# Optimization experiments

Hardware: AMD Instinct MI355X
Metric: run time of the kernel (lower is better)

## Reference

```python
import jax, jax.numpy as jnp
import numpy as np

N_NODES = 100000
N_EDGES = 4000000
CHANNELS = 64


def setup_inputs() -> dict:
    key = jax.random.key(0)
    k1, k2, k3, k4, k5 = jax.random.split(key, 5)
    x = jax.random.normal(k1, (N_NODES, CHANNELS), dtype=jnp.float32)
    sources = jax.random.randint(k2, (N_EDGES,), 0, N_NODES, dtype=jnp.int64)
    targets = jax.random.randint(k3, (N_EDGES,), 0, N_NODES, dtype=jnp.int64)
    norm = jax.random.uniform(k4, (N_NODES, 1), dtype=jnp.float32)
    # xavier_normal_ for a (64, 64) weight: std = sqrt(2 / (fan_in + fan_out))
    std = float(np.sqrt(2.0 / (CHANNELS + CHANNELS)))
    weight = jax.random.normal(k5, (CHANNELS, CHANNELS), dtype=jnp.float32) * std
    return {"x": x, "sources": sources, "targets": targets, "norm": norm, "weight": weight}


def reference(x, sources, targets, norm, weight):
    # x.index_add(0, targets, x[sources]) == x + segment_sum(x[sources], targets)
    messages = x[sources]  # [E, C] gather
    agg = x + jax.ops.segment_sum(messages, targets, num_segments=x.shape[0])  # [N, C]
    h = norm * agg  # per-node scale, norm broadcasts [N,1] over [N,C]
    return h @ weight  # [N, C]
```

## Files before the change

kernel.cpp:

```cpp
#include <hip/hip_runtime.h>


constexpr int C = 64;
constexpr int BN = 128;
constexpr int CHUNK2 = 8192;
constexpr int MAXB = 1024;
constexpr int NPASS = 7;
constexpr int BINS = BN * 8;
constexpr int ASTRIDE = 65;
constexpr int UNI = BN * ASTRIDE;
constexpr int TAILCAP = 65536;
constexpr int CSTR = 32;

__global__ __launch_bounds__(256) void init_kernel(
    int* __restrict__ cursor, int* __restrict__ tailcnt, int NB, int slot) {
  int i = blockIdx.x * 256 + threadIdx.x;
  if (i < NB) cursor[i * CSTR] = i * slot;
  if (i == NB) *tailcnt = 0;
}

__global__ __launch_bounds__(512) void binfused_kernel(
    const int* __restrict__ src, const int* __restrict__ tgt,
    int* __restrict__ gcursor, int* __restrict__ tailcnt,
    unsigned* __restrict__ tailrec, unsigned* __restrict__ recs,
    const float* __restrict__ x, unsigned* __restrict__ xb,
    int E, int NB, int slot, int binBlocks, int total8) {
  if ((int)blockIdx.x >= binBlocks) {
    int i = (blockIdx.x - binBlocks) * 512 + threadIdx.x;
    if (i < total8) {
      const float4* x4 = (const float4*)x;
      float4 a = x4[i * 2], bq = x4[i * 2 + 1];
      float f[8] = {a.x, a.y, a.z, a.w, bq.x, bq.y, bq.z, bq.w};
      unsigned w[4];
#pragma unroll
      for (int k = 0; k < 4; k++) {
        unsigned u0 = __float_as_uint(f[2 * k]);
        unsigned u1 = __float_as_uint(f[2 * k + 1]);
        u0 = (u0 + 0x7FFFu + ((u0 >> 16) & 1u)) >> 16;
        u1 = (u1 + 0x7FFFu + ((u1 >> 16) & 1u)) >> 16;
        w[k] = u0 | (u1 << 16);
      }
      ((uint4*)xb)[i] = make_uint4(w[0], w[1], w[2], w[3]);
    }
    return;
  }
  __shared__ unsigned rs[CHUNK2];
  __shared__ unsigned short sb[CHUNK2];
  __shared__ int hist[MAXB];
  __shared__ int gb[MAXB];
  __shared__ int cbase[MAXB];
  __shared__ int pre[512];
  int tid = threadIdx.x;
  int base = blockIdx.x * CHUNK2;
  int count = E - base; if (count > CHUNK2) count = CHUNK2;

  for (int i = tid; i < MAXB; i += 512) hist[i] = 0;
  __syncthreads();

  unsigned mrec[16];
  unsigned mbix[16];
  int nv = count >> 2;
  int rem = count & 3;
  const int4* s4 = (const int4*)(src + base);
  const int4* t4 = (const int4*)(tgt + base);
#pragma unroll
  for (int j = 0; j < 4; j++) {
    int i = tid + j * 512;
    if (i < nv) {
      int4 s = s4[i], t = t4[i];
      int b0 = t.x >> 7, b1 = t.y >> 7, b2 = t.z >> 7, b3 = t.w >> 7;
      mrec[4 * j + 0] = ((unsigned)s.x << 7) | (unsigned)(t.x & 127);
      mrec[4 * j + 1] = ((unsigned)s.y << 7) | (unsigned)(t.y & 127);
      mrec[4 * j + 2] = ((unsigned)s.z << 7) | (unsigned)(t.z & 127);
      mrec[4 * j + 3] = ((unsigned)s.w << 7) | (unsigned)(t.w & 127);
      mbix[4 * j + 0] = ((unsigned)b0 << 13) | (unsigned)atomicAdd(&hist[b0], 1);
      mbix[4 * j + 1] = ((unsigned)b1 << 13) | (unsigned)atomicAdd(&hist[b1], 1);
      mbix[4 * j + 2] = ((unsigned)b2 << 13) | (unsigned)atomicAdd(&hist[b2], 1);
      mbix[4 * j + 3] = ((unsigned)b3 << 13) | (unsigned)atomicAdd(&hist[b3], 1);
    } else {
#pragma unroll
      for (int k = 0; k < 4; k++) mbix[4 * j + k] = 0xFFFFFFFFu;
    }
  }
  unsigned trec = 0, tbix = 0xFFFFFFFFu;
  if (tid < rem) {
    int i = (nv << 2) + tid;
    int s = src[base + i], t = tgt[base + i];
    int b = t >> 7;
    trec = ((unsigned)s << 7) | (unsigned)(t & 127);
    tbix = ((unsigned)b << 13) | (unsigned)atomicAdd(&hist[b], 1);
  }
  __syncthreads();

  int c0 = hist[2 * tid], c1 = hist[2 * tid + 1];
  pre[tid] = c0 + c1;
  __syncthreads();
  for (int off = 1; off < 512; off <<= 1) {
    int v = pre[tid];
    int a = (tid >= off) ? pre[tid - off] : 0;
    __syncthreads();
    pre[tid] = v + a;
    __syncthreads();
  }
  {
    int run = pre[tid] - (c0 + c1);
    cbase[2 * tid] = run;
    cbase[2 * tid + 1] = run + c0;
  }
  if (2 * tid < NB && c0) gb[2 * tid] = atomicAdd(&gcursor[2 * tid * CSTR], c0);
  if (2 * tid + 1 < NB && c1)
    gb[2 * tid + 1] = atomicAdd(&gcursor[(2 * tid + 1) * CSTR], c1);
  __syncthreads();

#pragma unroll
  for (int j = 0; j < 16; j++) {
    unsigned v = mbix[j];
    if (v != 0xFFFFFFFFu) {
      int b = (int)(v >> 13);
      int pos = cbase[b] + (int)(v & 8191u);
      rs[pos] = mrec[j];
      sb[pos] = (unsigned short)b;
    }
  }
  if (tbix != 0xFFFFFFFFu) {
    int b = (int)(tbix >> 13);
    int pos = cbase[b] + (int)(tbix & 8191u);
    rs[pos] = trec;
    sb[pos] = (unsigned short)b;
  }
  __syncthreads();

  for (int i = tid; i < count; i += 512) {
    int b = (int)sb[i];
    int dest = gb[b] + (i - cbase[b]);
    if (dest < (b + 1) * slot) {
      recs[dest] = rs[i];
    } else {
      int tp = atomicAdd(tailcnt, 1);
      if (tp < TAILCAP) {
        tailrec[2 * tp] = rs[i];
        tailrec[2 * tp + 1] = (unsigned)b;
      }
    }
  }
}

__device__ __forceinline__ void acc8_bf16(float (&a)[8], uint4 v) {
  a[0] += __uint_as_float(v.x << 16);
  a[1] += __uint_as_float(v.x & 0xFFFF0000u);
  a[2] += __uint_as_float(v.y << 16);
  a[3] += __uint_as_float(v.y & 0xFFFF0000u);
  a[4] += __uint_as_float(v.z << 16);
  a[5] += __uint_as_float(v.z & 0xFFFF0000u);
  a[6] += __uint_as_float(v.w << 16);
  a[7] += __uint_as_float(v.w & 0xFFFF0000u);
}

__device__ __forceinline__ void acc8_f32(float (&a)[8], float4 u, float4 v) {
  a[0] += u.x; a[1] += u.y; a[2] += u.z; a[3] += u.w;
  a[4] += v.x; a[5] += v.y; a[6] += v.z; a[7] += v.w;
}

template <bool USE_BF16>
__global__ __launch_bounds__(512) void sortgather_kernel(
    const float* __restrict__ x, const unsigned* __restrict__ xb,
    const unsigned* __restrict__ recs, const int* __restrict__ cursor,
    const int* __restrict__ tailcnt, const unsigned* __restrict__ tailrec,
    const float* __restrict__ norm, const float* __restrict__ W,
    float* __restrict__ out, int N, int slot) {
  __shared__ int cnt[BINS];
  __shared__ int pre[512];
  __shared__ int nst[BINS + 1];
  __shared__ float uni[UNI];
  unsigned* sorted = (unsigned*)uni;
  float* accum = uni;
  int tid = threadIdx.x;
  int lane = tid & 63;
  int wave = tid >> 6;
  int b = blockIdx.x;
  int n0 = b * BN;
  int nn = N - n0; if (nn > BN) nn = BN;
  int beg = b * slot;
  int m = cursor[b * CSTR] - beg; if (m > slot) m = slot;
  int end = beg + m;

  unsigned myrec[16];
#pragma unroll
  for (int j = 0; j < 16; j++) {
    int r = beg + tid + j * 512;
    myrec[j] = (r < end) ? recs[r] : 0xFFFFFFFFu;
  }
  cnt[tid] = 0; cnt[tid + 512] = 0;
  __syncthreads();
#pragma unroll
  for (int j = 0; j < 16; j++) {
    unsigned rc = myrec[j];
    if (rc != 0xFFFFFFFFu) {
      int q = (int)(rc >> 21); if (q > 6) q = 6;
      atomicAdd(&cnt[((int)(rc & 127u) << 3) | q], 1);
    }
  }
  __syncthreads();
  int c0 = cnt[2 * tid], c1 = cnt[2 * tid + 1];
  pre[tid] = c0 + c1;
  __syncthreads();
  for (int off = 1; off < 512; off <<= 1) {
    int v = pre[tid];
    int a = (tid >= off) ? pre[tid - off] : 0;
    __syncthreads();
    pre[tid] = v + a;
    __syncthreads();
  }
  {
    int run = pre[tid] - (c0 + c1);
    nst[2 * tid] = run;
    nst[2 * tid + 1] = run + c0;
    cnt[2 * tid] = run;
    cnt[2 * tid + 1] = run + c0;
  }
  if (tid == 0) nst[BINS] = m;
  __syncthreads();
#pragma unroll
  for (int j = 0; j < 16; j++) {
    unsigned rc = myrec[j];
    if (rc != 0xFFFFFFFFu) {
      int q = (int)(rc >> 21); if (q > 6) q = 6;
      int p = atomicAdd(&cnt[((int)(rc & 127u) << 3) | q], 1);
      sorted[p] = rc >> 7;
    }
  }
  __syncthreads();

  int l7 = tid & 7;
  int g  = tid >> 3;
  int k0 = g, k1 = g + 64;
  bool has0 = k0 < nn, has1 = k1 < nn;
  const float4* x4 = (const float4*)x;
  const uint4* xb4 = (const uint4*)xb;

  float a0[8], a1[8];
  if (has0) {
    float4 u = x4[(n0 + k0) * 16 + l7 * 2], v = x4[(n0 + k0) * 16 + l7 * 2 + 1];
    a0[0] = u.x; a0[1] = u.y; a0[2] = u.z; a0[3] = u.w;
    a0[4] = v.x; a0[5] = v.y; a0[6] = v.z; a0[7] = v.w;
  } else {
#pragma unroll
    for (int j = 0; j < 8; j++) a0[j] = 0.0f;
  }
  if (has1) {
    float4 u = x4[(n0 + k1) * 16 + l7 * 2], v = x4[(n0 + k1) * 16 + l7 * 2 + 1];
    a1[0] = u.x; a1[1] = u.y; a1[2] = u.z; a1[3] = u.w;
    a1[4] = v.x; a1[5] = v.y; a1[6] = v.z; a1[7] = v.w;
  } else {
#pragma unroll
    for (int j = 0; j < 8; j++) a1[j] = 0.0f;
  }

  for (int p = 0; p < NPASS; p++) {
    if (has0) {
      int e = nst[k0 * 8 + p], ge = nst[k0 * 8 + p + 1];
      for (; e + 1 < ge; e += 2) {
        int s0 = (int)sorted[e], s1 = (int)sorted[e + 1];
        if (USE_BF16) {
          uint4 v0 = xb4[s0 * 8 + l7];
          uint4 v1 = xb4[s1 * 8 + l7];
          acc8_bf16(a0, v0); acc8_bf16(a0, v1);
        } else {
          float4 u0 = x4[s0 * 16 + l7 * 2], w0 = x4[s0 * 16 + l7 * 2 + 1];
          float4 u1 = x4[s1 * 16 + l7 * 2], w1 = x4[s1 * 16 + l7 * 2 + 1];
          acc8_f32(a0, u0, w0); acc8_f32(a0, u1, w1);
        }
      }
      if (e < ge) {
        int s = (int)sorted[e];
        if (USE_BF16) { uint4 v = xb4[s * 8 + l7]; acc8_bf16(a0, v); }
        else { acc8_f32(a0, x4[s * 16 + l7 * 2], x4[s * 16 + l7 * 2 + 1]); }
      }
    }
    if (has1) {
      int e = nst[k1 * 8 + p], ge = nst[k1 * 8 + p + 1];
      for (; e + 1 < ge; e += 2) {
        int s0 = (int)sorted[e], s1 = (int)sorted[e + 1];
        if (USE_BF16) {
          uint4 v0 = xb4[s0 * 8 + l7];
          uint4 v1 = xb4[s1 * 8 + l7];
          acc8_bf16(a1, v0); acc8_bf16(a1, v1);
        } else {
          float4 u0 = x4[s0 * 16 + l7 * 2], w0 = x4[s0 * 16 + l7 * 2 + 1];
          float4 u1 = x4[s1 * 16 + l7 * 2], w1 = x4[s1 * 16 + l7 * 2 + 1];
          acc8_f32(a1, u0, w0); acc8_f32(a1, u1, w1);
        }
      }
      if (e < ge) {
        int s = (int)sorted[e];
        if (USE_BF16) { uint4 v = xb4[s * 8 + l7]; acc8_bf16(a1, v); }
        else { acc8_f32(a1, x4[s * 16 + l7 * 2], x4[s * 16 + l7 * 2 + 1]); }
      }
    }
  }

  {
    int tc = *tailcnt; if (tc > TAILCAP) tc = TAILCAP;
    for (int r = 0; r < tc; r++) {
      if ((int)tailrec[2 * r + 1] != b) continue;
      unsigned rc = tailrec[2 * r];
      int tl = (int)(rc & 127u);
      if (tl == k0 || tl == k1) {
        int s = (int)(rc >> 7);
        if (USE_BF16) {
          uint4 v = xb4[s * 8 + l7];
          if (tl == k0) acc8_bf16(a0, v); else acc8_bf16(a1, v);
        } else {
          float4 u = x4[s * 16 + l7 * 2], w = x4[s * 16 + l7 * 2 + 1];
          if (tl == k0) acc8_f32(a0, u, w); else acc8_f32(a1, u, w);
        }
      }
    }
  }
  __syncthreads();

  if (has0) {
#pragma unroll
    for (int j = 0; j < 8; j++) accum[k0 * ASTRIDE + 8 * l7 + j] = a0[j];
  }
  if (has1) {
#pragma unroll
    for (int j = 0; j < 8; j++) accum[k1 * ASTRIDE + 8 * l7 + j] = a1[j];
  }
  __syncthreads();

  float wreg[C];
#pragma unroll
  for (int k = 0; k < C; k++) wreg[k] = W[k * C + lane];

  for (int i = wave; i < nn; i += 8) {
    int n = n0 + i;
    float a = accum[i * ASTRIDE + lane];
    float o = 0.0f;
#pragma unroll
    for (int c = 0; c < C; c++)
      o = fmaf(__shfl(a, c, 64), wreg[c], o);
    out[n * C + lane] = o * norm[n];
  }
}

extern "C" void kernel_launch(void* const* d_in, const int* in_sizes, int n_in,
                              void* d_out, int out_size, void* d_ws, size_t ws_size,
                              hipStream_t stream) {
  const float* x       = (const float*)d_in[0];
  const int*   sources = (const int*)d_in[1];
  const int*   targets = (const int*)d_in[2];
  const float* norm    = (const float*)d_in[3];
  const float* weight  = (const float*)d_in[4];
  float* out = (float*)d_out;

  int N = in_sizes[0] / C;
  int E = in_sizes[1];
  int NB = (N + BN - 1) / BN;

  size_t availw = ws_size / 4;
  size_t xw = (size_t)N * C / 2;
  size_t fixedw = (size_t)NB * CSTR + 1 + 2 * (size_t)TAILCAP;
  bool use_bf16; int slot;
  if (availw >= xw + fixedw + (size_t)NB * 8192) { use_bf16 = true; slot = 8192; }
  else if (availw >= xw + fixedw + (size_t)NB * 6144) { use_bf16 = true; slot = 6144; }
  else {
    use_bf16 = false;
    size_t s = (availw > fixedw) ? (availw - fixedw) / (size_t)NB : 0;
    slot = s > 8192 ? 8192 : (int)s;
  }

  unsigned* xb; int* cursor;
  if (use_bf16) {
    xb = (unsigned*)d_ws;
    cursor = (int*)d_ws + xw;
  } else {
    xb = nullptr;
    cursor = (int*)d_ws;
  }
  int* tailcnt = cursor + (size_t)NB * CSTR;
  unsigned* tailrec = (unsigned*)(tailcnt + 1);
  unsigned* recs = tailrec + 2 * (size_t)TAILCAP;

  int hb = (E + CHUNK2 - 1) / CHUNK2;
  int total8 = N * C / 8;
  int cvtBlocks = use_bf16 ? (total8 + 511) / 512 : 0;

  init_kernel<<<(NB + 256) / 256, 256, 0, stream>>>(cursor, tailcnt, NB, slot);
  binfused_kernel<<<hb + cvtBlocks, 512, 0, stream>>>(
      sources, targets, cursor, tailcnt, tailrec, recs, x, xb,
      E, NB, slot, hb, total8);
  if (use_bf16) {
    sortgather_kernel<true><<<NB, 512, 0, stream>>>(
        x, xb, recs, cursor, tailcnt, tailrec, norm, weight, out, N, slot);
  } else {
    sortgather_kernel<false><<<NB, 512, 0, stream>>>(
        x, xb, recs, cursor, tailcnt, tailrec, norm, weight, out, N, slot);
  }
}
```

Measured before the change: 284.0 us.

## Split bf16 convert kernel, scatter bins directly, make sortgather persistent

The bf16 conversion moves out of the fused binning kernel into its own grid-stride kernel. The binning kernel drops its shared-memory local sort and prefix scan and writes each record straight to its global slot, which cuts shared memory and barriers but makes the global writes less coalesced. The sortgather kernel becomes persistent, with 512 blocks looping over the 782 node tiles, which avoids one launch wave of blocks but gives an uneven two-pass tail. It also reloads the weight registers on every iteration.

```diff
diff --git a/kernel.cpp b/kernel.cpp
--- a/kernel.cpp
+++ b/kernel.cpp
@@ -11,6 +11,7 @@
 constexpr int UNI = BN * ASTRIDE;
 constexpr int TAILCAP = 65536;
 constexpr int CSTR = 32;
+constexpr int SGBLK = 512;
 
 __global__ __launch_bounds__(256) void init_kernel(
     int* __restrict__ cursor, int* __restrict__ tailcnt, int NB, int slot) {
@@ -19,37 +20,33 @@
   if (i == NB) *tailcnt = 0;
 }
 
-__global__ __launch_bounds__(512) void binfused_kernel(
+__global__ __launch_bounds__(256) void cvt_kernel(
+    const float* __restrict__ x, unsigned* __restrict__ xb, int total8) {
+  int stride = gridDim.x * 256;
+  for (int i = blockIdx.x * 256 + threadIdx.x; i < total8; i += stride) {
+    const float4* x4 = (const float4*)x;
+    float4 a = x4[i * 2], bq = x4[i * 2 + 1];
+    float f[8] = {a.x, a.y, a.z, a.w, bq.x, bq.y, bq.z, bq.w};
+    unsigned w[4];
+#pragma unroll
+    for (int k = 0; k < 4; k++) {
+      unsigned u0 = __float_as_uint(f[2 * k]);
+      unsigned u1 = __float_as_uint(f[2 * k + 1]);
+      u0 = (u0 + 0x7FFFu + ((u0 >> 16) & 1u)) >> 16;
+      u1 = (u1 + 0x7FFFu + ((u1 >> 16) & 1u)) >> 16;
+      w[k] = u0 | (u1 << 16);
+    }
+    ((uint4*)xb)[i] = make_uint4(w[0], w[1], w[2], w[3]);
+  }
+}
+
+__global__ __launch_bounds__(512) void bin_kernel(
     const int* __restrict__ src, const int* __restrict__ tgt,
     int* __restrict__ gcursor, int* __restrict__ tailcnt,
     unsigned* __restrict__ tailrec, unsigned* __restrict__ recs,
-    const float* __restrict__ x, unsigned* __restrict__ xb,
-    int E, int NB, int slot, int binBlocks, int total8) {
-  if ((int)blockIdx.x >= binBlocks) {
-    int i = (blockIdx.x - binBlocks) * 512 + threadIdx.x;
-    if (i < total8) {
-      const float4* x4 = (const float4*)x;
-      float4 a = x4[i * 2], bq = x4[i * 2 + 1];
-      float f[8] = {a.x, a.y, a.z, a.w, bq.x, bq.y, bq.z, bq.w};
-      unsigned w[4];
-#pragma unroll
-      for (int k = 0; k < 4; k++) {
-        unsigned u0 = __float_as_uint(f[2 * k]);
-        unsigned u1 = __float_as_uint(f[2 * k + 1]);
-        u0 = (u0 + 0x7FFFu + ((u0 >> 16) & 1u)) >> 16;
-        u1 = (u1 + 0x7FFFu + ((u1 >> 16) & 1u)) >> 16;
-        w[k] = u0 | (u1 << 16);
-      }
-      ((uint4*)xb)[i] = make_uint4(w[0], w[1], w[2], w[3]);
-    }
-    return;
-  }
-  __shared__ unsigned rs[CHUNK2];
-  __shared__ unsigned short sb[CHUNK2];
+    int E, int NB, int slot) {
   __shared__ int hist[MAXB];
   __shared__ int gb[MAXB];
-  __shared__ int cbase[MAXB];
-  __shared__ int pre[512];
   int tid = threadIdx.x;
   int base = blockIdx.x * CHUNK2;
   int count = E - base; if (count > CHUNK2) count = CHUNK2;
@@ -92,24 +89,10 @@
   }
   __syncthreads();
 
-  int c0 = hist[2 * tid], c1 = hist[2 * tid + 1];
-  pre[tid] = c0 + c1;
-  __syncthreads();
-  for (int off = 1; off < 512; off <<= 1) {
-    int v = pre[tid];
-    int a = (tid >= off) ? pre[tid - off] : 0;
-    __syncthreads();
-    pre[tid] = v + a;
-    __syncthreads();
-  }
-  {
-    int run = pre[tid] - (c0 + c1);
-    cbase[2 * tid] = run;
-    cbase[2 * tid + 1] = run + c0;
-  }
-  if (2 * tid < NB && c0) gb[2 * tid] = atomicAdd(&gcursor[2 * tid * CSTR], c0);
-  if (2 * tid + 1 < NB && c1)
-    gb[2 * tid + 1] = atomicAdd(&gcursor[(2 * tid + 1) * CSTR], c1);
+  for (int i = tid; i < NB; i += 512) {
+    int c = hist[i];
+    gb[i] = c ? atomicAdd(&gcursor[i * CSTR], c) : 0;
+  }
   __syncthreads();
 
 #pragma unroll
@@ -117,28 +100,27 @@
     unsigned v = mbix[j];
     if (v != 0xFFFFFFFFu) {
       int b = (int)(v >> 13);
-      int pos = cbase[b] + (int)(v & 8191u);
-      rs[pos] = mrec[j];
-      sb[pos] = (unsigned short)b;
+      int dest = gb[b] + (int)(v & 8191u);
+      if (dest < (b + 1) * slot) {
+        recs[dest] = mrec[j];
+      } else {
+        int tp = atomicAdd(tailcnt, 1);
+        if (tp < TAILCAP) {
+          tailrec[2 * tp] = mrec[j];
+          tailrec[2 * tp + 1] = (unsigned)b;
+        }
+      }
     }
   }
   if (tbix != 0xFFFFFFFFu) {
     int b = (int)(tbix >> 13);
-    int pos = cbase[b] + (int)(tbix & 8191u);
-    rs[pos] = trec;
-    sb[pos] = (unsigned short)b;
-  }
-  __syncthreads();
-
-  for (int i = tid; i < count; i += 512) {
-    int b = (int)sb[i];
-    int dest = gb[b] + (i - cbase[b]);
+    int dest = gb[b] + (int)(tbix & 8191u);
     if (dest < (b + 1) * slot) {
-      recs[dest] = rs[i];
+      recs[dest] = trec;
     } else {
       int tp = atomicAdd(tailcnt, 1);
       if (tp < TAILCAP) {
-        tailrec[2 * tp] = rs[i];
+        tailrec[2 * tp] = trec;
         tailrec[2 * tp + 1] = (unsigned)b;
       }
     }
@@ -167,7 +149,7 @@
     const unsigned* __restrict__ recs, const int* __restrict__ cursor,
     const int* __restrict__ tailcnt, const unsigned* __restrict__ tailrec,
     const float* __restrict__ norm, const float* __restrict__ W,
-    float* __restrict__ out, int N, int slot) {
+    float* __restrict__ out, int N, int slot, int NB) {
   __shared__ int cnt[BINS];
   __shared__ int pre[512];
   __shared__ int nst[BINS + 1];
@@ -177,170 +159,175 @@
   int tid = threadIdx.x;
   int lane = tid & 63;
   int wave = tid >> 6;
-  int b = blockIdx.x;
-  int n0 = b * BN;
-  int nn = N - n0; if (nn > BN) nn = BN;
-  int beg = b * slot;
-  int m = cursor[b * CSTR] - beg; if (m > slot) m = slot;
-  int end = beg + m;
-
-  unsigned myrec[16];
-#pragma unroll
-  for (int j = 0; j < 16; j++) {
-    int r = beg + tid + j * 512;
-    myrec[j] = (r < end) ? recs[r] : 0xFFFFFFFFu;
-  }
-  cnt[tid] = 0; cnt[tid + 512] = 0;
-  __syncthreads();
-#pragma unroll
-  for (int j = 0; j < 16; j++) {
-    unsigned rc = myrec[j];
-    if (rc != 0xFFFFFFFFu) {
-      int q = (int)(rc >> 21); if (q > 6) q = 6;
-      atomicAdd(&cnt[((int)(rc & 127u) << 3) | q], 1);
-    }
-  }
-  __syncthreads();
-  int c0 = cnt[2 * tid], c1 = cnt[2 * tid + 1];
-  pre[tid] = c0 + c1;
-  __syncthreads();
-  for (int off = 1; off < 512; off <<= 1) {
-    int v = pre[tid];
-    int a = (tid >= off) ? pre[tid - off] : 0;
-    __syncthreads();
-    pre[tid] = v + a;
-    __syncthreads();
-  }
-  {
-    int run = pre[tid] - (c0 + c1);
-    nst[2 * tid] = run;
-    nst[2 * tid + 1] = run + c0;
-    cnt[2 * tid] = run;
-    cnt[2 * tid + 1] = run + c0;
-  }
-  if (tid == 0) nst[BINS] = m;
-  __syncthreads();
-#pragma unroll
-  for (int j = 0; j < 16; j++) {
-    unsigned rc = myrec[j];
-    if (rc != 0xFFFFFFFFu) {
-      int q = (int)(rc >> 21); if (q > 6) q = 6;
-      int p = atomicAdd(&cnt[((int)(rc & 127u) << 3) | q], 1);
-      sorted[p] = rc >> 7;
-    }
-  }
-  __syncthreads();
-
-  int l7 = tid & 7;
-  int g  = tid >> 3;
-  int k0 = g, k1 = g + 64;
-  bool has0 = k0 < nn, has1 = k1 < nn;
-  const float4* x4 = (const float4*)x;
-  const uint4* xb4 = (const uint4*)xb;
-
-  float a0[8], a1[8];
-  if (has0) {
-    float4 u = x4[(n0 + k0) * 16 + l7 * 2], v = x4[(n0 + k0) * 16 + l7 * 2 + 1];
-    a0[0] = u.x; a0[1] = u.y; a0[2] = u.z; a0[3] = u.w;
-    a0[4] = v.x; a0[5] = v.y; a0[6] = v.z; a0[7] = v.w;
-  } else {
-#pragma unroll
-    for (int j = 0; j < 8; j++) a0[j] = 0.0f;
-  }
-  if (has1) {
-    float4 u = x4[(n0 + k1) * 16 + l7 * 2], v = x4[(n0 + k1) * 16 + l7 * 2 + 1];
-    a1[0] = u.x; a1[1] = u.y; a1[2] = u.z; a1[3] = u.w;
-    a1[4] = v.x; a1[5] = v.y; a1[6] = v.z; a1[7] = v.w;
-  } else {
-#pragma unroll
-    for (int j = 0; j < 8; j++) a1[j] = 0.0f;
-  }
-
-  for (int p = 0; p < NPASS; p++) {
+
+  for (int b = blockIdx.x; b < NB; b += SGBLK) {
+    int n0 = b * BN;
+    int nn = N - n0; if (nn > BN) nn = BN;
+    int beg = b * slot;
+    int m = cursor[b * CSTR] - beg; if (m > slot) m = slot;
+    int end = beg + m;
+
+    unsigned myrec[16];
+#pragma unroll
+    for (int j = 0; j < 16; j++) {
+      int r = beg + tid + j * 512;
+      myrec[j] = (r < end) ? recs[r] : 0xFFFFFFFFu;
+    }
+    cnt[tid] = 0; cnt[tid + 512] = 0;
+    __syncthreads();
+#pragma unroll
+    for (int j = 0; j < 16; j++) {
+      unsigned rc = myrec[j];
+      if (rc != 0xFFFFFFFFu) {
+        int q = (int)(rc >> 21); if (q > 6) q = 6;
+        atomicAdd(&cnt[((int)(rc & 127u) << 3) | q], 1);
+      }
+    }
+    __syncthreads();
+    int c0 = cnt[2 * tid], c1 = cnt[2 * tid + 1];
+    pre[tid] = c0 + c1;
+    __syncthreads();
+    for (int off = 1; off < 512; off <<= 1) {
+      int v = pre[tid];
+      int a = (tid >= off) ? pre[tid - off] : 0;
+      __syncthreads();
+      pre[tid] = v + a;
+      __syncthreads();
+    }
+    {
+      int run = pre[tid] - (c0 + c1);
+      nst[2 * tid] = run;
+      nst[2 * tid + 1] = run + c0;
+      cnt[2 * tid] = run;
+      cnt[2 * tid + 1] = run + c0;
+    }
+    if (tid == 0) nst[BINS] = m;
+    __syncthreads();
+#pragma unroll
+    for (int j = 0; j < 16; j++) {
+      unsigned rc = myrec[j];
+      if (rc != 0xFFFFFFFFu) {
+        int q = (int)(rc >> 21); if (q > 6) q = 6;
+        int p = atomicAdd(&cnt[((int)(rc & 127u) << 3) | q], 1);
+        sorted[p] = rc >> 7;
+      }
+    }
+    __syncthreads();
+
+    int l7 = tid & 7;
+    int g  = tid >> 3;
+    int k0 = g, k1 = g + 64;
+    bool has0 = k0 < nn, has1 = k1 < nn;
+    const float4* x4 = (const float4*)x;
+    const uint4* xb4 = (const uint4*)xb;
+
+    float a0[8], a1[8];
     if (has0) {
-      int e = nst[k0 * 8 + p], ge = nst[k0 * 8 + p + 1];
-      for (; e + 1 < ge; e += 2) {
-        int s0 = (int)sorted[e], s1 = (int)sorted[e + 1];
-        if (USE_BF16) {
-          uint4 v0 = xb4[s0 * 8 + l7];
-          uint4 v1 = xb4[s1 * 8 + l7];
-          acc8_bf16(a0, v0); acc8_bf16(a0, v1);
-        } else {
-          float4 u0 = x4[s0 * 16 + l7 * 2], w0 = x4[s0 * 16 + l7 * 2 + 1];
-          float4 u1 = x4[s1 * 16 + l7 * 2], w1 = x4[s1 * 16 + l7 * 2 + 1];
-          acc8_f32(a0, u0, w0); acc8_f32(a0, u1, w1);
-        }
-      }
-      if (e < ge) {
-        int s = (int)sorted[e];
-        if (USE_BF16) { uint4 v = xb4[s * 8 + l7]; acc8_bf16(a0, v); }
-        else { acc8_f32(a0, x4[s * 16 + l7 * 2], x4[s * 16 + l7 * 2 + 1]); }
-      }
+      float4 u = x4[(n0 + k0) * 16 + l7 * 2];
+      float4 v = x4[(n0 + k0) * 16 + l7 * 2 + 1];
+      a0[0] = u.x; a0[1] = u.y; a0[2] = u.z; a0[3] = u.w;
+      a0[4] = v.x; a0[5] = v.y; a0[6] = v.z; a0[7] = v.w;
+    } else {
+#pragma unroll
+      for (int j = 0; j < 8; j++) a0[j] = 0.0f;
     }
     if (has1) {
-      int e = nst[k1 * 8 + p], ge = nst[k1 * 8 + p + 1];
-      for (; e + 1 < ge; e += 2) {
-        int s0 = (int)sorted[e], s1 = (int)sorted[e + 1];
-        if (USE_BF16) {
-          uint4 v0 = xb4[s0 * 8 + l7];
-          uint4 v1 = xb4[s1 * 8 + l7];
-          acc8_bf16(a1, v0); acc8_bf16(a1, v1);
-        } else {
-          float4 u0 = x4[s0 * 16 + l7 * 2], w0 = x4[s0 * 16 + l7 * 2 + 1];
-          float4 u1 = x4[s1 * 16 + l7 * 2], w1 = x4[s1 * 16 + l7 * 2 + 1];
-          acc8_f32(a1, u0, w0); acc8_f32(a1, u1, w1);
-        }
-      }
-      if (e < ge) {
-        int s = (int)sorted[e];
-        if (USE_BF16) { uint4 v = xb4[s * 8 + l7]; acc8_bf16(a1, v); }
-        else { acc8_f32(a1, x4[s * 16 + l7 * 2], x4[s * 16 + l7 * 2 + 1]); }
-      }
-    }
-  }
-
-  {
-    int tc = *tailcnt; if (tc > TAILCAP) tc = TAILCAP;
-    for (int r = 0; r < tc; r++) {
-      if ((int)tailrec[2 * r + 1] != b) continue;
-      unsigned rc = tailrec[2 * r];
-      int tl = (int)(rc & 127u);
-      if (tl == k0 || tl == k1) {
-        int s = (int)(rc >> 7);
-        if (USE_BF16) {
-          uint4 v = xb4[s * 8 + l7];
-          if (tl == k0) acc8_bf16(a0, v); else acc8_bf16(a1, v);
-        } else {
-          float4 u = x4[s * 16 + l7 * 2], w = x4[s * 16 + l7 * 2 + 1];
-          if (tl == k0) acc8_f32(a0, u, w); else acc8_f32(a1, u, w);
-        }
-      }
-    }
-  }
-  __syncthreads();
-
-  if (has0) {
-#pragma unroll
-    for (int j = 0; j < 8; j++) accum[k0 * ASTRIDE + 8 * l7 + j] = a0[j];
-  }
-  if (has1) {
-#pragma unroll
-    for (int j = 0; j < 8; j++) accum[k1 * ASTRIDE + 8 * l7 + j] = a1[j];
-  }
-  __syncthreads();
-
-  float wreg[C];
-#pragma unroll
-  for (int k = 0; k < C; k++) wreg[k] = W[k * C + lane];
-
-  for (int i = wave; i < nn; i += 8) {
-    int n = n0 + i;
-    float a = accum[i * ASTRIDE + lane];
-    float o = 0.0f;
-#pragma unroll
-    for (int c = 0; c < C; c++)
-      o = fmaf(__shfl(a, c, 64), wreg[c], o);
-    out[n * C + lane] = o * norm[n];
+      float4 u = x4[(n0 + k1) * 16 + l7 * 2];
+      float4 v = x4[(n0 + k1) * 16 + l7 * 2 + 1];
+      a1[0] = u.x; a1[1] = u.y; a1[2] = u.z; a1[3] = u.w;
+      a1[4] = v.x; a1[5] = v.y; a1[6] = v.z; a1[7] = v.w;
+    } else {
+#pragma unroll
+      for (int j = 0; j < 8; j++) a1[j] = 0.0f;
+    }
+
+    for (int p = 0; p < NPASS; p++) {
+      if (has0) {
+        int e = nst[k0 * 8 + p], ge = nst[k0 * 8 + p + 1];
+        for (; e + 1 < ge; e += 2) {
+          int s0 = (int)sorted[e], s1 = (int)sorted[e + 1];
+          if (USE_BF16) {
+            uint4 v0 = xb4[s0 * 8 + l7];
+            uint4 v1 = xb4[s1 * 8 + l7];
+            acc8_bf16(a0, v0); acc8_bf16(a0, v1);
+          } else {
+            float4 u0 = x4[s0 * 16 + l7 * 2], w0 = x4[s0 * 16 + l7 * 2 + 1];
+            float4 u1 = x4[s1 * 16 + l7 * 2], w1 = x4[s1 * 16 + l7 * 2 + 1];
+            acc8_f32(a0, u0, w0); acc8_f32(a0, u1, w1);
+          }
+        }
+        if (e < ge) {
+          int s = (int)sorted[e];
+          if (USE_BF16) { uint4 v = xb4[s * 8 + l7]; acc8_bf16(a0, v); }
+          else { acc8_f32(a0, x4[s * 16 + l7 * 2], x4[s * 16 + l7 * 2 + 1]); }
+        }
+      }
+      if (has1) {
+        int e = nst[k1 * 8 + p], ge = nst[k1 * 8 + p + 1];
+        for (; e + 1 < ge; e += 2) {
+          int s0 = (int)sorted[e], s1 = (int)sorted[e + 1];
+          if (USE_BF16) {
+            uint4 v0 = xb4[s0 * 8 + l7];
+            uint4 v1 = xb4[s1 * 8 + l7];
+            acc8_bf16(a1, v0); acc8_bf16(a1, v1);
+          } else {
+            float4 u0 = x4[s0 * 16 + l7 * 2], w0 = x4[s0 * 16 + l7 * 2 + 1];
+            float4 u1 = x4[s1 * 16 + l7 * 2], w1 = x4[s1 * 16 + l7 * 2 + 1];
+            acc8_f32(a1, u0, w0); acc8_f32(a1, u1, w1);
+          }
+        }
+        if (e < ge) {
+          int s = (int)sorted[e];
+          if (USE_BF16) { uint4 v = xb4[s * 8 + l7]; acc8_bf16(a1, v); }
+          else { acc8_f32(a1, x4[s * 16 + l7 * 2], x4[s * 16 + l7 * 2 + 1]); }
+        }
+      }
+    }
+
+    {
+      int tc = *tailcnt; if (tc > TAILCAP) tc = TAILCAP;
+      for (int r = 0; r < tc; r++) {
+        if ((int)tailrec[2 * r + 1] != b) continue;
+        unsigned rc = tailrec[2 * r];
+        int tl = (int)(rc & 127u);
+        if (tl == k0 || tl == k1) {
+          int s = (int)(rc >> 7);
+          if (USE_BF16) {
+            uint4 v = xb4[s * 8 + l7];
+            if (tl == k0) acc8_bf16(a0, v); else acc8_bf16(a1, v);
+          } else {
+            float4 u = x4[s * 16 + l7 * 2], w = x4[s * 16 + l7 * 2 + 1];
+            if (tl == k0) acc8_f32(a0, u, w); else acc8_f32(a1, u, w);
+          }
+        }
+      }
+    }
+    __syncthreads();
+
+    if (has0) {
+#pragma unroll
+      for (int j = 0; j < 8; j++) accum[k0 * ASTRIDE + 8 * l7 + j] = a0[j];
+    }
+    if (has1) {
+#pragma unroll
+      for (int j = 0; j < 8; j++) accum[k1 * ASTRIDE + 8 * l7 + j] = a1[j];
+    }
+    __syncthreads();
+
+    float wreg[C];
+#pragma unroll
+    for (int k = 0; k < C; k++) wreg[k] = W[k * C + lane];
+
+    for (int i = wave; i < nn; i += 8) {
+      int n = n0 + i;
+      float a = accum[i * ASTRIDE + lane];
+      float o = 0.0f;
+#pragma unroll
+      for (int c = 0; c < C; c++)
+        o = fmaf(__shfl(a, c, 64), wreg[c], o);
+      out[n * C + lane] = o * norm[n];
+    }
+    __syncthreads();
   }
 }
 
@@ -384,17 +371,21 @@
 
   int hb = (E + CHUNK2 - 1) / CHUNK2;
   int total8 = N * C / 8;
-  int cvtBlocks = use_bf16 ? (total8 + 511) / 512 : 0;
 
   init_kernel<<<(NB + 256) / 256, 256, 0, stream>>>(cursor, tailcnt, NB, slot);
-  binfused_kernel<<<hb + cvtBlocks, 512, 0, stream>>>(
-      sources, targets, cursor, tailcnt, tailrec, recs, x, xb,
-      E, NB, slot, hb, total8);
   if (use_bf16) {
-    sortgather_kernel<true><<<NB, 512, 0, stream>>>(
-        x, xb, recs, cursor, tailcnt, tailrec, norm, weight, out, N, slot);
+    int cvtGrid = (total8 + 255) / 256;
+    if (cvtGrid > 2048) cvtGrid = 2048;
+    cvt_kernel<<<cvtGrid, 256, 0, stream>>>(x, xb, total8);
+  }
+  bin_kernel<<<hb, 512, 0, stream>>>(
+      sources, targets, cursor, tailcnt, tailrec, recs, E, NB, slot);
+  int sg = NB < SGBLK ? NB : SGBLK;
+  if (use_bf16) {
+    sortgather_kernel<true><<<sg, 512, 0, stream>>>(
+        x, xb, recs, cursor, tailcnt, tailrec, norm, weight, out, N, slot, NB);
   } else {
-    sortgather_kernel<false><<<NB, 512, 0, stream>>>(
-        x, xb, recs, cursor, tailcnt, tailrec, norm, weight, out, N, slot);
-  }
-}
+    sortgather_kernel<false><<<sg, 512, 0, stream>>>(
+        x, xb, recs, cursor, tailcnt, tailrec, norm, weight, out, N, slot, NB);
+  }
+}
```

After: 420.6 us. 48.1% more time.
